# Performance work log

Hardware: AMD Instinct MI355X
Metric: run time of the kernel (lower is better)

## Reference

```python
import jax, jax.numpy as jnp
import numpy as np

NUM_Q = 1000
B, T = 64, 100
DK, DV, N = 128, 128, 128

def setup_inputs() -> dict:
    key = jax.random.key(0)
    ks = jax.random.split(key, 12)
    return {
        "q": jax.random.randint(ks[0], (B, T), 0, NUM_Q),
        "r": jax.random.randint(ks[1], (B, T), 0, 2),
        "k_emb": jax.random.normal(ks[2], (NUM_Q, DK), jnp.float32) * 0.1,
        "v_emb": jax.random.normal(ks[3], (2 * NUM_Q, DV), jnp.float32) * 0.1,
        "Mk": jax.random.normal(ks[4], (DK, N), jnp.float32) * 0.1,
        "Mv0": jax.random.normal(ks[5], (N, DV), jnp.float32) * 0.1,
        "f_W": jax.random.normal(ks[6], (2 * DK, DK), jnp.float32) * 0.05,
        "f_b": jnp.zeros((DK,), jnp.float32),
        "p_W": jax.random.normal(ks[7], (DK, 1), jnp.float32) * 0.05,
        "p_b": jnp.zeros((1,), jnp.float32),
        "e_W": jax.random.normal(ks[8], (DV, DV), jnp.float32) * 0.05,
        "e_b": jnp.zeros((DV,), jnp.float32),
        "a_W": jax.random.normal(ks[9], (DV, DV), jnp.float32) * 0.05,
        "a_b": jnp.zeros((DV,), jnp.float32),
    }

def reference(q, r, k_emb, v_emb, Mk, Mv0, f_W, f_b, p_W, p_b, e_W, e_b, a_W, a_b):
    num_q = k_emb.shape[0]
    qr = q + num_q * r                                    # [B,T]
    K = k_emb[q].transpose(1, 0, 2)                       # [T,B,DK]
    V = v_emb[qr].transpose(1, 0, 2)                      # [T,B,DV]
    Mvt0 = jnp.broadcast_to(Mv0, (q.shape[0],) + Mv0.shape)  # [B,N,DV]

    def step(Mvt, kv):
        kt, vt = kv                                       # [B,DK],[B,DV]
        wt = jax.nn.softmax(kt @ Mk, axis=-1)             # [B,N] attention weights
        rt = jnp.einsum('bn,bnd->bd', wt, Mvt)            # memory read
        ft = jnp.tanh(jnp.concatenate([rt, kt], axis=-1) @ f_W + f_b)
        pt = jax.nn.sigmoid(ft @ p_W + p_b)               # [B,1]
        et = jax.nn.sigmoid(vt @ e_W + e_b)               # erase gate [B,DV]
        at = jnp.tanh(vt @ a_W + a_b)                     # add vector [B,DV]
        w_ = wt[:, :, None]                               # [B,N,1]
        Mvt = Mvt * (1.0 - w_ * et[:, None, :]) + w_ * at[:, None, :]
        return Mvt, (pt, Mvt)

    _, (p, Mv) = jax.lax.scan(step, Mvt0, (K, V))         # p: [T,B,1], Mv: [T,B,N,DV]
    p = p.reshape(-1, 1)                                  # cat over time, dim=0 -> [T*B,1]
    Mv = Mv.reshape(-1, Mv.shape[-2], Mv.shape[-1])       # [T*B,N,DV]
    return p, Mv
```

## Files before the change

kernel.cpp:

```cpp
#include <hip/hip_runtime.h>
#include <stdint.h>
#include <stddef.h>


constexpr int B = 64;
constexpr int T = 100;
constexpr int D = 128;
constexpr int NUM_Q = 1000;
constexpr int G = 4;
constexpr int CG = 4;
constexpr int BT = B * T;
constexpr int WSTRIDE = BT * D;
constexpr int NTILES = 16;

typedef float v4f __attribute__((ext_vector_type(4)));

__device__ __forceinline__ float sigmoidf_(float x) {
  return 1.0f / (1.0f + __expf(-x));
}

__global__ __launch_bounds__(128) void kernelA(
    const int* __restrict__ q, const int* __restrict__ r,
    const float* __restrict__ k_emb, const float* __restrict__ v_emb,
    const float* __restrict__ Mk,
    const float* __restrict__ f_W, const float* __restrict__ f_b,
    const float* __restrict__ e_W, const float* __restrict__ e_b,
    const float* __restrict__ a_W, const float* __restrict__ a_b,
    float* __restrict__ ws_w, float* __restrict__ ws_e,
    float* __restrict__ ws_a, float* __restrict__ ws_f)
{
  const int tid = threadIdx.x;
  const int b  = blockIdx.x / (T / G);
  const int tg = blockIdx.x % (T / G);
  const int tbase = tg * G;

  __shared__ float kt[G][D];
  __shared__ float vt[G][D];
  __shared__ float redm[2], reds[2];

  #pragma unroll
  for (int g = 0; g < G; ++g) {
    int idx = b * T + tbase + g;
    int qi  = q[idx];
    int qri = qi + NUM_Q * r[idx];
    kt[g][tid] = k_emb[qi * D + tid];
    vt[g][tid] = v_emb[qri * D + tid];
  }
  __syncthreads();

  float lg[G], se[G], sa[G], sf[G];
  #pragma unroll
  for (int g = 0; g < G; ++g) { lg[g] = 0.f; se[g] = 0.f; sa[g] = 0.f; sf[g] = 0.f; }

  #pragma unroll 4
  for (int k = 0; k < D; ++k) {
    float mk = Mk[k * D + tid];
    float ew = e_W[k * D + tid];
    float aw = a_W[k * D + tid];
    float fw = f_W[(D + k) * D + tid];
    #pragma unroll
    for (int g = 0; g < G; ++g) {
      float kk = kt[g][k];
      float vv = vt[g][k];
      lg[g] = fmaf(kk, mk, lg[g]);
      se[g] = fmaf(vv, ew, se[g]);
      sa[g] = fmaf(vv, aw, sa[g]);
      sf[g] = fmaf(kk, fw, sf[g]);
    }
  }

  const float eb = e_b[tid];
  const float ab = a_b[tid];
  const float fb = f_b[tid];

  for (int g = 0; g < G; ++g) {
    float v = lg[g];
    #pragma unroll
    for (int s = 32; s > 0; s >>= 1) v = fmaxf(v, __shfl_xor(v, s));
    if ((tid & 63) == 0) redm[tid >> 6] = v;
    __syncthreads();
    float mx = fmaxf(redm[0], redm[1]);
    float ex = __expf(lg[g] - mx);
    v = ex;
    #pragma unroll
    for (int s = 32; s > 0; s >>= 1) v += __shfl_xor(v, s);
    if ((tid & 63) == 0) reds[tid >> 6] = v;
    __syncthreads();
    float sm = reds[0] + reds[1];

    int idx = (b * T + tbase + g) * D + tid;
    ws_w[idx] = ex / sm;
    ws_e[idx] = sigmoidf_(se[g] + eb);
    ws_a[idx] = tanhf(sa[g] + ab);
    ws_f[idx] = sf[g] + fb;
  }
}

__global__ __launch_bounds__(256) void kernelB(
    const float* __restrict__ Mv0,
    const float* __restrict__ ws_w, const float* __restrict__ ws_e,
    const float* __restrict__ ws_a,
    float* __restrict__ out_Mv, float* __restrict__ ws_rt)
{
  const int j = blockIdx.x;
  const int b  = ((j & 7) << 3) | ((j >> 3) & 7);
  const int nt = j >> 6;
  const int tid = threadIdx.x;
  const int nrow = tid >> 5;
  const int dgrp = tid & 31;
  const int n  = nt * 8 + nrow;
  const int d0 = dgrp * 4;
  const int wave = tid >> 6;
  const int lane = tid & 63;

  __shared__ float part[2][4][32][4];

  float m[4];
  #pragma unroll
  for (int i = 0; i < 4; ++i) m[i] = Mv0[n * D + d0 + i];

  const float*  pw = ws_w + (size_t)(b * T) * D + n;
  const float4* pe = (const float4*)(ws_e + (size_t)(b * T) * D + d0);
  const float4* pa = (const float4*)(ws_a + (size_t)(b * T) * D + d0);

  float  wv = pw[0];
  float4 ev = pe[0];
  float4 av = pa[0];

  for (int t = 0; t < T; ++t) {
    const int tn = (t + 1 < T) ? (t + 1) : t;
    float  wn = pw[(size_t)tn * D];
    float4 en = pe[(size_t)tn * 32];
    float4 an = pa[(size_t)tn * 32];

    float prx = wv * m[0], pry = wv * m[1], prz = wv * m[2], prw = wv * m[3];
    prx += __shfl_xor(prx, 32);
    pry += __shfl_xor(pry, 32);
    prz += __shfl_xor(prz, 32);
    prw += __shfl_xor(prw, 32);
    if (lane < 32) {
      float4 pr4 = make_float4(prx, pry, prz, prw);
      *(float4*)&part[t & 1][wave][dgrp][0] = pr4;
    }

    float ee[4] = {ev.x, ev.y, ev.z, ev.w};
    float aa[4] = {av.x, av.y, av.z, av.w};
    #pragma unroll
    for (int i = 0; i < 4; ++i) {
      m[i] = m[i] * (1.0f - wv * ee[i]) + wv * aa[i];
    }

    size_t obase = ((size_t)(t * B + b) * D + n) * D + d0;
    v4f o0 = {m[0], m[1], m[2], m[3]};
    __builtin_nontemporal_store(o0, (v4f*)(out_Mv + obase));

    __syncthreads();
    if (tid < D) {
      float s = part[t & 1][0][tid >> 2][tid & 3]
              + part[t & 1][1][tid >> 2][tid & 3]
              + part[t & 1][2][tid >> 2][tid & 3]
              + part[t & 1][3][tid >> 2][tid & 3];
      ws_rt[((size_t)(b * T + t) * NTILES + nt) * D + tid] = s;
    }

    wv = wn; ev = en; av = an;
  }
}

__global__ __launch_bounds__(128) void kernelC(
    const float* __restrict__ f_W,
    const float* __restrict__ p_W,
    const float* __restrict__ p_b,
    const float* __restrict__ ws_f, const float* __restrict__ ws_rt,
    float* __restrict__ out_p)
{
  const int grp = blockIdx.x;
  const int b  = grp / (T / CG);
  const int tg = grp % (T / CG);
  const int t0 = tg * CG;
  const int bt0 = b * T + t0;
  const int tid = threadIdx.x;

  __shared__ float rsh[CG][D];
  __shared__ float wred[CG][2];

  float fa[CG];
  #pragma unroll
  for (int g = 0; g < CG; ++g) {
    const float* prt = ws_rt + (size_t)(bt0 + g) * (NTILES * D);
    float rt = 0.f;
    #pragma unroll
    for (int nt = 0; nt < NTILES; ++nt) rt += prt[nt * D + tid];
    rsh[g][tid] = rt;
    fa[g] = ws_f[(bt0 + g) * D + tid];
  }
  __syncthreads();

  #pragma unroll 4
  for (int d2 = 0; d2 < D; ++d2) {
    float fw = f_W[d2 * D + tid];
    #pragma unroll
    for (int g = 0; g < CG; ++g) fa[g] = fmaf(rsh[g][d2], fw, fa[g]);
  }

  const float pw = p_W[tid];
  #pragma unroll
  for (int g = 0; g < CG; ++g) {
    float v = tanhf(fa[g]) * pw;
    #pragma unroll
    for (int s = 32; s > 0; s >>= 1) v += __shfl_xor(v, s);
    if ((tid & 63) == 0) wred[g][tid >> 6] = v;
  }
  __syncthreads();
  if (tid < CG) {
    float pt = sigmoidf_(wred[tid][0] + wred[tid][1] + p_b[0]);
    out_p[(t0 + tid) * B + b] = pt;
  }
}

extern "C" void kernel_launch(void* const* d_in, const int* in_sizes, int n_in,
                              void* d_out, int out_size, void* d_ws, size_t ws_size,
                              hipStream_t stream)
{
  const int* q = (const int*)d_in[0];
  const int* r = (const int*)d_in[1];
  const float* k_emb = (const float*)d_in[2];
  const float* v_emb = (const float*)d_in[3];
  const float* Mk   = (const float*)d_in[4];
  const float* Mv0  = (const float*)d_in[5];
  const float* f_W  = (const float*)d_in[6];
  const float* f_b  = (const float*)d_in[7];
  const float* p_W  = (const float*)d_in[8];
  const float* p_b  = (const float*)d_in[9];
  const float* e_W  = (const float*)d_in[10];
  const float* e_b  = (const float*)d_in[11];
  const float* a_W  = (const float*)d_in[12];
  const float* a_b  = (const float*)d_in[13];

  float* ws   = (float*)d_ws;
  float* ws_w = ws;
  float* ws_e = ws + (size_t)WSTRIDE;
  float* ws_a = ws + (size_t)2 * WSTRIDE;
  float* ws_f = ws + (size_t)3 * WSTRIDE;
  float* ws_rt = ws + (size_t)4 * WSTRIDE;

  float* out    = (float*)d_out;
  float* out_p  = out;
  float* out_Mv = out + BT;

  hipLaunchKernelGGL(kernelA, dim3(B * (T / G)), dim3(D), 0, stream,
                     q, r, k_emb, v_emb, Mk, f_W, f_b, e_W, e_b, a_W, a_b,
                     ws_w, ws_e, ws_a, ws_f);
  hipLaunchKernelGGL(kernelB, dim3(B * NTILES), dim3(256), 0, stream,
                     Mv0, ws_w, ws_e, ws_a, out_Mv, ws_rt);
  hipLaunchKernelGGL(kernelC, dim3(B * (T / CG)), dim3(D), 0, stream,
                     f_W, p_W, p_b, ws_f, ws_rt, out_p);
}
```

Baseline: 504.3 us.

## Split memory scan into separate store kernel and read-reduction kernel

The recurrent memory update is split in two. One kernel only evolves Mv and streams it to the output, with no per-step barrier or shared-memory reduction. A second kernel recomputes the same recurrence with a layout where each wave owns 4 columns across all 128 rows, and produces the full memory read with wave shuffles, so no partial-tile reduction is needed later. This removes the per-timestep __syncthreads and the 16-way partial sums, at the cost of doing the recurrence twice and adding a launch.

```diff
diff --git a/kernel.cpp b/kernel.cpp
--- a/kernel.cpp
+++ b/kernel.cpp
@@ -11,7 +11,6 @@
 constexpr int CG = 4;
 constexpr int BT = B * T;
 constexpr int WSTRIDE = BT * D;
-constexpr int NTILES = 16;
 
 typedef float v4f __attribute__((ext_vector_type(4)));
 
@@ -96,11 +95,11 @@
   }
 }
 
-__global__ __launch_bounds__(256) void kernelB(
+__global__ __launch_bounds__(256) void kernelB1(
     const float* __restrict__ Mv0,
     const float* __restrict__ ws_w, const float* __restrict__ ws_e,
     const float* __restrict__ ws_a,
-    float* __restrict__ out_Mv, float* __restrict__ ws_rt)
+    float* __restrict__ out_Mv)
 {
   const int j = blockIdx.x;
   const int b  = ((j & 7) << 3) | ((j >> 3) & 7);
@@ -110,10 +109,6 @@
   const int dgrp = tid & 31;
   const int n  = nt * 8 + nrow;
   const int d0 = dgrp * 4;
-  const int wave = tid >> 6;
-  const int lane = tid & 63;
-
-  __shared__ float part[2][4][32][4];
 
   float m[4];
   #pragma unroll
@@ -133,16 +128,6 @@
     float4 en = pe[(size_t)tn * 32];
     float4 an = pa[(size_t)tn * 32];
 
-    float prx = wv * m[0], pry = wv * m[1], prz = wv * m[2], prw = wv * m[3];
-    prx += __shfl_xor(prx, 32);
-    pry += __shfl_xor(pry, 32);
-    prz += __shfl_xor(prz, 32);
-    prw += __shfl_xor(prw, 32);
-    if (lane < 32) {
-      float4 pr4 = make_float4(prx, pry, prz, prw);
-      *(float4*)&part[t & 1][wave][dgrp][0] = pr4;
-    }
-
     float ee[4] = {ev.x, ev.y, ev.z, ev.w};
     float aa[4] = {av.x, av.y, av.z, av.w};
     #pragma unroll
@@ -154,13 +139,65 @@
     v4f o0 = {m[0], m[1], m[2], m[3]};
     __builtin_nontemporal_store(o0, (v4f*)(out_Mv + obase));
 
-    __syncthreads();
-    if (tid < D) {
-      float s = part[t & 1][0][tid >> 2][tid & 3]
-              + part[t & 1][1][tid >> 2][tid & 3]
-              + part[t & 1][2][tid >> 2][tid & 3]
-              + part[t & 1][3][tid >> 2][tid & 3];
-      ws_rt[((size_t)(b * T + t) * NTILES + nt) * D + tid] = s;
+    wv = wn; ev = en; av = an;
+  }
+}
+
+__global__ __launch_bounds__(256) void kernelB2(
+    const float* __restrict__ Mv0,
+    const float* __restrict__ ws_w, const float* __restrict__ ws_e,
+    const float* __restrict__ ws_a,
+    float* __restrict__ ws_rt)
+{
+  const int j = blockIdx.x;
+  const int b  = ((j & 7) << 3) | ((j >> 3) & 7);
+  const int dq = j >> 6;
+  const int tid = threadIdx.x;
+  const int wave = tid >> 6;
+  const int lane = tid & 63;
+  const int d0 = dq * 16 + wave * 4;
+  const int n0 = 2 * lane;
+
+  float m0[4], m1[4];
+  #pragma unroll
+  for (int i = 0; i < 4; ++i) {
+    m0[i] = Mv0[n0 * D + d0 + i];
+    m1[i] = Mv0[(n0 + 1) * D + d0 + i];
+  }
+
+  const float2* pw = (const float2*)(ws_w + (size_t)(b * T) * D) + lane;
+  const float4* pe = (const float4*)(ws_e + (size_t)(b * T) * D + d0);
+  const float4* pa = (const float4*)(ws_a + (size_t)(b * T) * D + d0);
+
+  float2 wv = pw[0];
+  float4 ev = pe[0];
+  float4 av = pa[0];
+
+  for (int t = 0; t < T; ++t) {
+    const int tn = (t + 1 < T) ? (t + 1) : t;
+    float2 wn = pw[(size_t)tn * 64];
+    float4 en = pe[(size_t)tn * 32];
+    float4 an = pa[(size_t)tn * 32];
+
+    float pr[4];
+    #pragma unroll
+    for (int i = 0; i < 4; ++i) pr[i] = wv.x * m0[i] + wv.y * m1[i];
+    #pragma unroll
+    for (int s = 1; s < 64; s <<= 1) {
+      #pragma unroll
+      for (int i = 0; i < 4; ++i) pr[i] += __shfl_xor(pr[i], s);
+    }
+    if (lane == 0) {
+      v4f r4 = {pr[0], pr[1], pr[2], pr[3]};
+      *(v4f*)(ws_rt + (size_t)(b * T + t) * D + d0) = r4;
+    }
+
+    float ee[4] = {ev.x, ev.y, ev.z, ev.w};
+    float aa[4] = {av.x, av.y, av.z, av.w};
+    #pragma unroll
+    for (int i = 0; i < 4; ++i) {
+      m0[i] = m0[i] * (1.0f - wv.x * ee[i]) + wv.x * aa[i];
+      m1[i] = m1[i] * (1.0f - wv.y * ee[i]) + wv.y * aa[i];
     }
 
     wv = wn; ev = en; av = an;
@@ -187,11 +224,7 @@
   float fa[CG];
   #pragma unroll
   for (int g = 0; g < CG; ++g) {
-    const float* prt = ws_rt + (size_t)(bt0 + g) * (NTILES * D);
-    float rt = 0.f;
-    #pragma unroll
-    for (int nt = 0; nt < NTILES; ++nt) rt += prt[nt * D + tid];
-    rsh[g][tid] = rt;
+    rsh[g][tid] = ws_rt[(size_t)(bt0 + g) * D + tid];
     fa[g] = ws_f[(bt0 + g) * D + tid];
   }
   __syncthreads();
@@ -251,8 +284,10 @@
   hipLaunchKernelGGL(kernelA, dim3(B * (T / G)), dim3(D), 0, stream,
                      q, r, k_emb, v_emb, Mk, f_W, f_b, e_W, e_b, a_W, a_b,
                      ws_w, ws_e, ws_a, ws_f);
-  hipLaunchKernelGGL(kernelB, dim3(B * NTILES), dim3(256), 0, stream,
-                     Mv0, ws_w, ws_e, ws_a, out_Mv, ws_rt);
+  hipLaunchKernelGGL(kernelB1, dim3(B * 16), dim3(256), 0, stream,
+                     Mv0, ws_w, ws_e, ws_a, out_Mv);
+  hipLaunchKernelGGL(kernelB2, dim3(B * 8), dim3(256), 0, stream,
+                     Mv0, ws_w, ws_e, ws_a, ws_rt);
   hipLaunchKernelGGL(kernelC, dim3(B * (T / CG)), dim3(D), 0, stream,
                      f_W, p_W, p_b, ws_f, ws_rt, out_p);
 }
```

Measured after the change: 553.7 us. 1.1x slower.
